# Optimization experiments

Measured on AMD Instinct MI355X. Metric: run time of the kernel, lower is better.

The kernel has to match this reference:

```python
import jax, jax.numpy as jnp
import numpy as np

B, T, H, N = 4, 2048, 16, 64  # batch, seq, heads, head_size (RWKV standard N=64)


def setup_inputs() -> dict:
    key = jax.random.key(0)
    ks = jax.random.split(key, 5)
    r = jax.random.normal(ks[0], (B, T, H, N), jnp.float32)
    k = jax.random.normal(ks[1], (B, T, H, N), jnp.float32)
    v = jax.random.normal(ks[2], (B, T, H, N), jnp.float32)
    w = jax.random.normal(ks[3], (B, T, H, N), jnp.float32)  # raw decay logits
    u = jax.random.normal(ks[4], (H, N), jnp.float32)         # per-head bonus
    return {"r": r, "k": k, "v": v, "w": w, "u": u}


def _wkv_scan(r, k, v, w, u):
    # RWKV-6 fused recurrent WKV.
    # decay in (0,1): exp(-exp(w)) per RWKV-6 parameterization
    decay = jnp.exp(-jnp.exp(w))  # [B,T,H,N]
    # time-major for lax.scan: [T,B,H,N]
    rt = jnp.moveaxis(r, 1, 0)
    kt = jnp.moveaxis(k, 1, 0)
    vt = jnp.moveaxis(v, 1, 0)
    dt = jnp.moveaxis(decay, 1, 0)
    S0 = jnp.zeros((r.shape[0], r.shape[2], r.shape[3], r.shape[3]), r.dtype)  # [B,H,N,N]

    ub = u[None]  # [1,H,N] broadcast over batch; key index i gets bonus

    def step(S, x):
        r_t, k_t, v_t, d_t = x  # each [B,H,N]
        kv = k_t[..., :, None] * v_t[..., None, :]  # [B,H,N,N] outer product
        # o_j = sum_i r_i * (S_ij + u_i * kv_ij)
        o = jnp.einsum('bhi,bhij->bhj', r_t, S + ub[..., None] * kv)
        S_new = d_t[..., None] * S + kv  # per-channel decay on key axis
        return S_new, o

    _, o = jax.lax.scan(step, S0, (rt, kt, vt, dt))  # o: [T,B,H,N]
    return jnp.moveaxis(o, 0, 1)  # [B,T,H,N]


def reference(r, k, v, w, u):
    return _wkv_scan(r, k, v, w, u)
```

## Files before the change

kernel.cpp:

```cpp
#include <hip/hip_runtime.h>
#include <math.h>


namespace {
constexpr int B = 4, T = 2048, H = 16, N = 64;
constexpr int BH = B * H;
constexpr int NG = 32;
constexpr int TC = 64;
constexpr int LDP = 72;

typedef __attribute__((ext_vector_type(8))) short s8v;
typedef __attribute__((ext_vector_type(4))) float f4v;

#define MFMA16(a, b, c) __builtin_amdgcn_mfma_f32_16x16x32_bf16((a), (b), (c), 0, 0, 0)

__device__ __forceinline__ unsigned short cv(float f) {
    union { float f; unsigned u; } x; x.f = f;
    unsigned r = x.u + 0x7FFFu + ((x.u >> 16) & 1u);
    return (unsigned short)(r >> 16);
}

__device__ __forceinline__ float bfhi(unsigned u) {
    union { unsigned u; float f; } x; x.u = u & 0xFFFF0000u; return x.f;
}
__device__ __forceinline__ float bflo(unsigned u) {
    union { unsigned u; float f; } x; x.u = u << 16; return x.f;
}

__device__ __forceinline__ int sw(int row, int col) {
    return row * LDP + col;
}

__device__ __forceinline__ s8v frag8(const unsigned short* buf, int row_base, int k_base) {
    const int l = threadIdx.x & 63;
    return *(const s8v*)&buf[sw(row_base + (l & 15), k_base + 8 * (l >> 4))];
}

template<int PHASE>
__global__ __launch_bounds__(256, 4)
void k13(const float* __restrict__ rp, const float* __restrict__ kp,
         const float* __restrict__ vp, const float* __restrict__ wp,
         const float* __restrict__ up,
         const unsigned short* __restrict__ S0g,
         unsigned short* __restrict__ Lg, float* __restrict__ Ag,
         float* __restrict__ out)
{
    __shared__ unsigned short sA[64 * LDP];
    __shared__ unsigned short sB[64 * LDP];
    __shared__ unsigned short sVT[64 * LDP];
    __shared__ unsigned short sST[64 * LDP];
    __shared__ float spans[4 * 64];
    unsigned short* const sAm = sA;

    const int blk = blockIdx.x;
    const int g   = blk & (NG - 1);
    const int bh  = blk / NG;
    const int b   = bh / H, h = bh - b * H;
    const int wv  = threadIdx.x >> 6;
    const int ln  = threadIdx.x & 63;

    const int stride = H * N;
    const int base_w = ((b * T + g * TC + wv * 16) * H + h) * N + ln;
    const int cb = (bh * NG + g) * (N * N);

    float ci[16];
    float k_[16], r_[16];
    {
        float run = 0.f;
#pragma unroll
        for (int tt = 0; tt < 16; ++tt) {
            const int a = base_w + tt * stride;
            run += __expf(wp[a]);
            ci[tt] = run;
            k_[tt] = kp[a];
            if (PHASE == 1) r_[tt] = rp[a];
        }
        spans[wv * 64 + ln] = run;
    }
#pragma unroll
    for (int half = 0; half < 2; ++half) {
        s8v pk;
#pragma unroll
        for (int e = 0; e < 8; ++e)
            pk[e] = (short)cv(vp[base_w + (half * 8 + e) * stride]);
        *(s8v*)&sVT[sw(ln, wv * 16 + half * 8)] = pk;
    }
    if (PHASE == 1) {
        *(s8v*)&sST[sw(ln, wv * 16)] =
            *(const s8v*)&S0g[cb + ln * 64 + wv * 16];
        *(s8v*)&sST[sw(ln, wv * 16 + 8)] =
            *(const s8v*)&S0g[cb + ln * 64 + wv * 16 + 8];
    }
    __syncthreads();
    const float sp0 = spans[0 * 64 + ln], sp1 = spans[1 * 64 + ln];
    const float sp2 = spans[2 * 64 + ln], sp3 = spans[3 * 64 + ln];
    const float offW = (wv > 0 ? sp0 : 0.f) + (wv > 1 ? sp1 : 0.f) + (wv > 2 ? sp2 : 0.f);
    const float ctot = sp0 + sp1 + sp2 + sp3;

    if (PHASE == 0) {
        s8v p0, p1;
#pragma unroll
        for (int tt = 0; tt < 16; ++tt) {
            const unsigned short v16 =
                cv(k_[tt] * __expf(-(ctot - (offW + ci[tt]))));
            if (tt < 8) p0[tt] = (short)v16; else p1[tt - 8] = (short)v16;
        }
        *(s8v*)&sA[sw(ln, wv * 16)]     = p0;
        *(s8v*)&sA[sw(ln, wv * 16 + 8)] = p1;
        __syncthreads();
#pragma unroll
        for (int jb = 0; jb < 4; ++jb) {
            f4v acc = {0.f, 0.f, 0.f, 0.f};
            acc = MFMA16(frag8(sA, wv * 16, 0),  frag8(sVT, jb * 16, 0),  acc);
            acc = MFMA16(frag8(sA, wv * 16, 32), frag8(sVT, jb * 16, 32), acc);
            const int i0 = wv * 16 + (ln >> 4) * 4;
            const int j  = jb * 16 + (ln & 15);
            uint2 wsto;
            wsto.x = (unsigned)cv(acc[0]) | ((unsigned)cv(acc[1]) << 16);
            wsto.y = (unsigned)cv(acc[2]) | ((unsigned)cv(acc[3]) << 16);
            *(uint2*)&Lg[cb + j * 64 + i0] = wsto;
        }
        if (wv == 0) Ag[(bh * NG + g) * 64 + ln] = __expf(-ctot);
        return;
    }

    const float uln = up[h * 64 + ln];
    const int cc = ln & 15;

    f4v accD = {0.f, 0.f, 0.f, 0.f};
#pragma unroll
    for (int tt = 0; tt < 16; ++tt) sB[sw(wv * 16 + tt, ln)] = cv(k_[tt]);
#pragma unroll
    for (int tt = 0; tt < 16; ++tt) sA[sw(wv * 16 + tt, ln)] = cv(r_[tt]);
    {
        f4v tmp = {0.f, 0.f, 0.f, 0.f};
        tmp = MFMA16(frag8(sA, wv * 16, 0),  frag8(sB, wv * 16, 0),  tmp);
        tmp = MFMA16(frag8(sA, wv * 16, 32), frag8(sB, wv * 16, 32), tmp);
#pragma unroll
        for (int q = 0; q < 4; ++q) {
            const int tt = (ln >> 4) * 4 + q;
            if (tt == cc + 1 && (tt & 1)) accD[q] += tmp[q];
        }
    }
#pragma unroll
    for (int tt = 0; tt < 16; ++tt) sA[sw(wv * 16 + tt, ln)] = cv(r_[tt] * uln);
    {
        f4v tmp = {0.f, 0.f, 0.f, 0.f};
        tmp = MFMA16(frag8(sA, wv * 16, 0),  frag8(sB, wv * 16, 0),  tmp);
        tmp = MFMA16(frag8(sA, wv * 16, 32), frag8(sB, wv * 16, 32), tmp);
#pragma unroll
        for (int q = 0; q < 4; ++q) {
            const int tt = (ln >> 4) * 4 + q;
            if (tt == cc) accD[q] += tmp[q];
        }
    }
#pragma unroll
    for (int L = 1; L < 4; ++L) {
#pragma unroll
        for (int tt = 0; tt < 16; ++tt) {
            const int btl = (tt >> L) << L;
            const int bsl = btl + (1 << L);
            const float cT  = (tt == 0) ? 0.f : ci[tt - 1];
            const float cBt = (btl == 0) ? 0.f : ci[btl - 1];
            const float cBs = ci[bsl - 1];
            sA[sw(wv * 16 + tt, ln)] = cv(r_[tt] * __expf(-(cT - cBt)));
            sB[sw(wv * 16 + tt, ln)] = cv(k_[tt] * __expf(-(cBs - ci[tt])));
        }
        f4v tmp = {0.f, 0.f, 0.f, 0.f};
        tmp = MFMA16(frag8(sA, wv * 16, 0),  frag8(sB, wv * 16, 0),  tmp);
        tmp = MFMA16(frag8(sA, wv * 16, 32), frag8(sB, wv * 16, 32), tmp);
#pragma unroll
        for (int q = 0; q < 4; ++q) {
            const int tt = (ln >> 4) * 4 + q;
            if (((tt >> L) == ((cc >> L) + 1)) && (((tt >> L) & 1) != 0))
                accD[q] += tmp[q];
        }
    }

#pragma unroll
    for (int tt = 0; tt < 16; ++tt) {
        const float cT = (tt == 0) ? 0.f : ci[tt - 1];
        sA[sw(wv * 16 + tt, ln)] = cv(r_[tt] * __expf(-cT));
        sB[sw(wv * 16 + tt, ln)] = cv(k_[tt] * __expf(-(ci[15] - ci[tt])));
    }
    __syncthreads();
    f4v accL4 = {0.f, 0.f, 0.f, 0.f};
    if (wv == 1 || wv == 3) {
        accL4 = MFMA16(frag8(sA, wv * 16, 0),  frag8(sB, (wv - 1) * 16, 0),  accL4);
        accL4 = MFMA16(frag8(sA, wv * 16, 32), frag8(sB, (wv - 1) * 16, 32), accL4);
    }
    __syncthreads();

#pragma unroll
    for (int tt = 0; tt < 16; ++tt) {
        if (wv >= 2) {
            const float cT = (tt == 0) ? 0.f : ci[tt - 1];
            const float d  = (wv == 2) ? cT : (cT + sp2);
            sA[sw(wv * 16 + tt, ln)] = cv(r_[tt] * __expf(-d));
        } else {
            const float d = (wv == 0) ? (sp0 + sp1 - ci[tt]) : (sp1 - ci[tt]);
            sB[sw(wv * 16 + tt, ln)] = cv(k_[tt] * __expf(-d));
        }
    }
    __syncthreads();
    f4v acc50 = {0.f, 0.f, 0.f, 0.f}, acc51 = {0.f, 0.f, 0.f, 0.f};
    if (wv >= 2) {
        acc50 = MFMA16(frag8(sA, wv * 16, 0),  frag8(sB, 0, 0),   acc50);
        acc50 = MFMA16(frag8(sA, wv * 16, 32), frag8(sB, 0, 32),  acc50);
        acc51 = MFMA16(frag8(sA, wv * 16, 0),  frag8(sB, 16, 0),  acc51);
        acc51 = MFMA16(frag8(sA, wv * 16, 32), frag8(sB, 16, 32), acc51);
    }

#pragma unroll
    for (int tt = 0; tt < 16; ++tt) {
        const float cT = (tt == 0) ? 0.f : ci[tt - 1];
        sA[sw(wv * 16 + tt, ln)] = cv(r_[tt] * __expf(-(offW + cT)));
    }
    f4v accO[4];
#pragma unroll
    for (int jb = 0; jb < 4; ++jb) {
        f4v a = {0.f, 0.f, 0.f, 0.f};
        a = MFMA16(frag8(sA, wv * 16, 0),  frag8(sST, jb * 16, 0),  a);
        a = MFMA16(frag8(sA, wv * 16, 32), frag8(sST, jb * 16, 32), a);
        accO[jb] = a;
    }

#pragma unroll
    for (int q = 0; q < 4; ++q) {
        const int tt = (ln >> 4) * 4 + q;
        sAm[sw(wv * 16 + tt, wv * 16 + cc)] = cv(accD[q]);
    }
    if (wv == 1 || wv == 3) {
#pragma unroll
        for (int q = 0; q < 4; ++q) {
            const int tt = (ln >> 4) * 4 + q;
            sAm[sw(wv * 16 + tt, (wv - 1) * 16 + cc)] = cv(accL4[q]);
        }
    }
    if (wv >= 2) {
#pragma unroll
        for (int q = 0; q < 4; ++q) {
            const int tt = (ln >> 4) * 4 + q;
            sAm[sw(wv * 16 + tt, cc)]      = cv(acc50[q]);
            sAm[sw(wv * 16 + tt, 16 + cc)] = cv(acc51[q]);
        }
    }
    if (wv == 0 || wv == 2) {
#pragma unroll
        for (int q = 0; q < 4; ++q) {
            const int tt = (ln >> 4) * 4 + q;
            sAm[sw(wv * 16 + tt, (wv + 1) * 16 + cc)] = 0;
        }
    }

#pragma unroll
    for (int jb = 0; jb < 4; ++jb) {
        f4v a = accO[jb];
        a = MFMA16(frag8(sAm, wv * 16, 0), frag8(sVT, jb * 16, 0), a);
        if (wv >= 2)
            a = MFMA16(frag8(sAm, wv * 16, 32), frag8(sVT, jb * 16, 32), a);
#pragma unroll
        for (int q = 0; q < 4; ++q) {
            const int t = g * TC + wv * 16 + (ln >> 4) * 4 + q;
            out[((b * T + t) * H + h) * N + jb * 16 + (ln & 15)] = a[q];
        }
    }
}

__global__ __launch_bounds__(256)
void k2_scan(unsigned short* __restrict__ L, const float* __restrict__ A)
{
    const int tid = blockIdx.x * 256 + threadIdx.x;
    const int i4 = tid & 15;
    const int j  = (tid >> 4) & 63;
    const int bh = tid >> 10;

    const int lstride = N * N;
    int lidx = bh * NG * lstride + j * 64 + i4 * 4;
    int aidx = bh * NG * N + i4 * 4;

    float s0 = 0.f, s1 = 0.f, s2 = 0.f, s3 = 0.f;
    for (int g = 0; g < NG; ++g) {
        const uint2  lw = *(const uint2*)&L[lidx];
        const float4 a  = *(const float4*)&A[aidx];
        uint2 wsto;
        wsto.x = (unsigned)cv(s0) | ((unsigned)cv(s1) << 16);
        wsto.y = (unsigned)cv(s2) | ((unsigned)cv(s3) << 16);
        *(uint2*)&L[lidx] = wsto;
        s0 = fmaf(a.x, s0, bflo(lw.x));
        s1 = fmaf(a.y, s1, bfhi(lw.x));
        s2 = fmaf(a.z, s2, bflo(lw.y));
        s3 = fmaf(a.w, s3, bfhi(lw.y));
        lidx += lstride;
        aidx += N;
    }
}

__global__ __launch_bounds__(64, 2)
void k_seq(const float* __restrict__ rp, const float* __restrict__ kp,
           const float* __restrict__ vp, const float* __restrict__ wp,
           const float* __restrict__ up, float* __restrict__ out)
{
    const int bh = blockIdx.x;
    const int b = bh / H, h = bh - b * H;
    const int j = threadIdx.x;

    float S[N];
#pragma unroll
    for (int i = 0; i < N; ++i) S[i] = 0.f;

    const int stride = H * N;
    int base = ((b * T) * H + h) * N;
    const int ubase = h * N;

#pragma unroll 1
    for (int tt = 0; tt < T; ++tt) {
        const float vj = vp[base + j];
        const int row = base;
        float sr = 0.f, o0 = 0.f, o1 = 0.f;
#pragma unroll
        for (int i = 0; i < N; ++i) {
            const float ki = kp[row + i];
            const float di = __expf(-__expf(wp[row + i]));
            const float ri = rp[row + i];
            sr = fmaf(ri * up[ubase + i], ki, sr);
            if (i & 1) o1 = fmaf(ri, S[i], o1);
            else       o0 = fmaf(ri, S[i], o0);
            S[i] = fmaf(di, S[i], ki * vj);
        }
        out[base + j] = fmaf(sr, vj, o0 + o1);
        base += stride;
    }
}

}

extern "C" void kernel_launch(void* const* d_in, const int* in_sizes, int n_in,
                              void* d_out, int out_size, void* d_ws, size_t ws_size,
                              hipStream_t stream)
{
    const float* r = (const float*)d_in[0];
    const float* k = (const float*)d_in[1];
    const float* v = (const float*)d_in[2];
    const float* w = (const float*)d_in[3];
    const float* u = (const float*)d_in[4];
    float* out = (float*)d_out;

    const size_t l_elems = (size_t)BH * NG * N * N;
    const size_t a_elems = (size_t)BH * NG * N;
    const size_t ws_need = l_elems * sizeof(unsigned short)
                         + a_elems * sizeof(float);

    if (ws_size >= ws_need) {
        unsigned short* L = (unsigned short*)d_ws;
        float* A = (float*)(L + l_elems);
        k13<0><<<BH * NG, 256, 0, stream>>>(r, k, v, w, u, nullptr, L, A, nullptr);
        k2_scan<<<(BH * N * 16) / 256, 256, 0, stream>>>(L, A);
        k13<1><<<BH * NG, 256, 0, stream>>>(r, k, v, w, u, L, nullptr, nullptr, out);
    } else {
        k_seq<<<BH, 64, 0, stream>>>(r, k, v, w, u, out);
    }
}
```

Measured before the change: 77.17 us.

## Store chunk states i-major, widen scan parallelism, alias state tile onto sB

Phase 0 now writes the per-chunk state contributions in [i][j] order instead of [j][i], so each thread stores four scattered bf16 values. The scan kernel is rewritten to match: each thread handles one key row i and a pair of j columns, which doubles the thread count and reads one decay scalar per row. Phase 1 drops the separate sST shared buffer by aliasing it onto sB, then loads the state late, after extra barriers, and transposes it during the load. The intent is lower LDS use (better occupancy) and more parallelism in the scan, at the cost of uncoalesced 2-byte stores in phase 0 and two added __syncthreads in phase 1.

```diff
diff --git a/kernel.cpp b/kernel.cpp
--- a/kernel.cpp
+++ b/kernel.cpp
@@ -48,9 +48,9 @@
     __shared__ unsigned short sA[64 * LDP];
     __shared__ unsigned short sB[64 * LDP];
     __shared__ unsigned short sVT[64 * LDP];
-    __shared__ unsigned short sST[64 * LDP];
     __shared__ float spans[4 * 64];
     unsigned short* const sAm = sA;
+    unsigned short* const sST = sB;
 
     const int blk = blockIdx.x;
     const int g   = blk & (NG - 1);
@@ -85,12 +85,6 @@
             pk[e] = (short)cv(vp[base_w + (half * 8 + e) * stride]);
         *(s8v*)&sVT[sw(ln, wv * 16 + half * 8)] = pk;
     }
-    if (PHASE == 1) {
-        *(s8v*)&sST[sw(ln, wv * 16)] =
-            *(const s8v*)&S0g[cb + ln * 64 + wv * 16];
-        *(s8v*)&sST[sw(ln, wv * 16 + 8)] =
-            *(const s8v*)&S0g[cb + ln * 64 + wv * 16 + 8];
-    }
     __syncthreads();
     const float sp0 = spans[0 * 64 + ln], sp1 = spans[1 * 64 + ln];
     const float sp2 = spans[2 * 64 + ln], sp3 = spans[3 * 64 + ln];
@@ -115,10 +109,9 @@
             acc = MFMA16(frag8(sA, wv * 16, 32), frag8(sVT, jb * 16, 32), acc);
             const int i0 = wv * 16 + (ln >> 4) * 4;
             const int j  = jb * 16 + (ln & 15);
-            uint2 wsto;
-            wsto.x = (unsigned)cv(acc[0]) | ((unsigned)cv(acc[1]) << 16);
-            wsto.y = (unsigned)cv(acc[2]) | ((unsigned)cv(acc[3]) << 16);
-            *(uint2*)&Lg[cb + j * 64 + i0] = wsto;
+#pragma unroll
+            for (int q = 0; q < 4; ++q)
+                Lg[cb + (i0 + q) * 64 + j] = cv(acc[q]);
         }
         if (wv == 0) Ag[(bh * NG + g) * 64 + ln] = __expf(-ctot);
         return;
@@ -216,6 +209,20 @@
         const float cT = (tt == 0) ? 0.f : ci[tt - 1];
         sA[sw(wv * 16 + tt, ln)] = cv(r_[tt] * __expf(-(offW + cT)));
     }
+    __syncthreads();
+
+    {
+        s8v p0, p1;
+#pragma unroll
+        for (int e = 0; e < 8; ++e) {
+            p0[e] = (short)S0g[cb + (wv * 16 + e) * 64 + ln];
+            p1[e] = (short)S0g[cb + (wv * 16 + 8 + e) * 64 + ln];
+        }
+        *(s8v*)&sST[sw(ln, wv * 16)]     = p0;
+        *(s8v*)&sST[sw(ln, wv * 16 + 8)] = p1;
+    }
+    __syncthreads();
+
     f4v accO[4];
 #pragma unroll
     for (int jb = 0; jb < 4; ++jb) {
@@ -271,26 +278,22 @@
 void k2_scan(unsigned short* __restrict__ L, const float* __restrict__ A)
 {
     const int tid = blockIdx.x * 256 + threadIdx.x;
-    const int i4 = tid & 15;
-    const int j  = (tid >> 4) & 63;
-    const int bh = tid >> 10;
-
-    const int lstride = N * N;
-    int lidx = bh * NG * lstride + j * 64 + i4 * 4;
-    int aidx = bh * NG * N + i4 * 4;
-
-    float s0 = 0.f, s1 = 0.f, s2 = 0.f, s3 = 0.f;
+    const int j2 = tid & 31;
+    const int i  = (tid >> 5) & 63;
+    const int bh = tid >> 11;
+
+    unsigned* Lu = (unsigned*)L;
+    const int lstride = N * N / 2;
+    int lidx = (bh * NG) * lstride + i * 32 + j2;
+    int aidx = (bh * NG) * N + i;
+
+    float s0 = 0.f, s1 = 0.f;
     for (int g = 0; g < NG; ++g) {
-        const uint2  lw = *(const uint2*)&L[lidx];
-        const float4 a  = *(const float4*)&A[aidx];
-        uint2 wsto;
-        wsto.x = (unsigned)cv(s0) | ((unsigned)cv(s1) << 16);
-        wsto.y = (unsigned)cv(s2) | ((unsigned)cv(s3) << 16);
-        *(uint2*)&L[lidx] = wsto;
-        s0 = fmaf(a.x, s0, bflo(lw.x));
-        s1 = fmaf(a.y, s1, bfhi(lw.x));
-        s2 = fmaf(a.z, s2, bflo(lw.y));
-        s3 = fmaf(a.w, s3, bfhi(lw.y));
+        const unsigned lw = Lu[lidx];
+        const float a = A[aidx];
+        Lu[lidx] = (unsigned)cv(s0) | ((unsigned)cv(s1) << 16);
+        s0 = fmaf(a, s0, bflo(lw));
+        s1 = fmaf(a, s1, bfhi(lw));
         lidx += lstride;
         aidx += N;
     }
@@ -355,7 +358,7 @@
         unsigned short* L = (unsigned short*)d_ws;
         float* A = (float*)(L + l_elems);
         k13<0><<<BH * NG, 256, 0, stream>>>(r, k, v, w, u, nullptr, L, A, nullptr);
-        k2_scan<<<(BH * N * 16) / 256, 256, 0, stream>>>(L, A);
+        k2_scan<<<(BH * N * N / 2) / 256, 256, 0, stream>>>(L, A);
         k13<1><<<BH * NG, 256, 0, stream>>>(r, k, v, w, u, L, nullptr, nullptr, out);
     } else {
         k_seq<<<BH, 64, 0, stream>>>(r, k, v, w, u, out);
```

New measurement: 71.82 us. -6.9%, faster.
